# Optimization experiments

Hardware: AMD Instinct MI355X
Metric: run time of the kernel (lower is better)

## Reference

```python
import jax, jax.numpy as jnp
import numpy as np

D_MODEL = 1024
NUM_HEADS = 16
NUM_KV_HEADS = 4
D_K = D_MODEL // NUM_HEADS          # 64
GROUP = NUM_HEADS // NUM_KV_HEADS   # 4
D_KV = D_MODEL // GROUP             # 256


def setup_inputs() -> dict:
    key = jax.random.key(0)
    ks = jax.random.split(key, 12)
    B, S = 2, 2048
    sc = 0.02
    return {
        "query": jax.random.normal(ks[0], (B, S, D_MODEL), jnp.float32),
        "key": jax.random.normal(ks[1], (B, S, D_MODEL), jnp.float32),
        "value": jax.random.normal(ks[2], (B, S, D_MODEL), jnp.float32),
        "w_q": jax.random.normal(ks[3], (D_MODEL, D_MODEL), jnp.float32) * sc,
        "b_q": jnp.zeros((D_MODEL,), jnp.float32),
        "w_k": jax.random.normal(ks[4], (D_KV, D_MODEL), jnp.float32) * sc,
        "b_k": jnp.zeros((D_KV,), jnp.float32),
        "w_v": jax.random.normal(ks[5], (D_KV, D_MODEL), jnp.float32) * sc,
        "b_v": jnp.zeros((D_KV,), jnp.float32),
        "w_o": jax.random.normal(ks[6], (D_MODEL, D_MODEL), jnp.float32) * sc,
        "b_o": jnp.zeros((D_MODEL,), jnp.float32),
    }


def reference(query, key, value, w_q, b_q, w_k, b_k, w_v, b_v, w_o, b_o):
    B, S, _ = query.shape
    # projections (torch Linear: x @ W.T + b)
    Q = query @ w_q.T + b_q            # [B,S,d_model]
    K = key @ w_k.T + b_k              # [B,S,d_kv]
    V = value @ w_v.T + b_v            # [B,S,d_kv]
    # [B, Hkv, G, S, Dk] for Q; [B, Hkv, S, Dk] for K/V.
    # repeat_interleave(group, dim=1) on K/V == sharing each KV head across
    # its group of query heads, so we contract without duplicating K/V.
    Q = Q.reshape(B, S, NUM_KV_HEADS, GROUP, D_K).transpose(0, 2, 3, 1, 4)
    K = K.reshape(B, S, NUM_KV_HEADS, D_K).transpose(0, 2, 1, 3)
    V = V.reshape(B, S, NUM_KV_HEADS, D_K).transpose(0, 2, 1, 3)
    scale = 1.0 / jnp.sqrt(jnp.asarray(D_K, Q.dtype))
    scores = jnp.einsum('bhgsd,bhtd->bhgst', Q, K) * scale  # [B,Hkv,G,S,S]
    attn = jax.nn.softmax(scores, axis=-1)
    out = jnp.einsum('bhgst,bhtd->bhgsd', attn, V)          # [B,Hkv,G,S,Dk]
    # -> [B,S,Hkv*G*Dk] = [B,S,d_model]
    out = out.transpose(0, 3, 1, 2, 4).reshape(B, S, D_MODEL)
    return out @ w_o.T + b_o
```

## Files before the change

kernel.cpp:

```cpp
#include <hip/hip_runtime.h>
#include <hip/hip_bf16.h>
#include <stdint.h>

typedef unsigned short u16;
typedef unsigned int   u32;
typedef short s16x8 __attribute__((ext_vector_type(8)));
typedef u16   u16x4 __attribute__((ext_vector_type(4)));
typedef u16   u16x8 __attribute__((ext_vector_type(8)));
typedef u32   u32x2 __attribute__((ext_vector_type(2)));
typedef u32   u32x4 __attribute__((ext_vector_type(4)));
typedef float f32x4  __attribute__((ext_vector_type(4)));
typedef float f32x16 __attribute__((ext_vector_type(16)));
typedef float f4     __attribute__((ext_vector_type(4)));

#define MFMA(a,b,c)   __builtin_amdgcn_mfma_f32_16x16x32_bf16((a),(b),(c),0,0,0)
#define MFMA32(a,b,c) __builtin_amdgcn_mfma_f32_32x32x16_bf16((a),(b),(c),0,0,0)

__device__ __forceinline__ u16 f2b(float f){
  union { float f; unsigned u; } v; v.f = f;
  unsigned r = v.u + 0x7fffu + ((v.u >> 16) & 1u);
  return (u16)(r >> 16);
}

__device__ __forceinline__ u32 cvtpk(float lo, float hi){
  u32 r;
  asm("v_cvt_pk_bf16_f32 %0, %1, %2" : "=v"(r) : "v"(lo), "v"(hi));
  return r;
}

__device__ __forceinline__ float exp2h(float x){
  float r;
  asm("v_exp_f32 %0, %1" : "=v"(r) : "v"(x));
  return r;
}

__device__ __forceinline__ void gll16(const void* g, void* l){
  __builtin_amdgcn_global_load_lds(
      (const __attribute__((address_space(1))) void*)g,
      (__attribute__((address_space(3))) void*)l, 16, 0, 0);
}

__global__ __launch_bounds__(256) void wcast(const float* __restrict__ wq,
                                             const float* __restrict__ wk,
                                             const float* __restrict__ wv,
                                             const float* __restrict__ wo,
                                             u16* dq, u16* dk, u16* dv, u16* dov){
  int e = (blockIdx.x * 256 + threadIdx.x) * 4;
  const float* s; u16* d; int off;
  if      (e < 1048576){ s = wq; d = dq;  off = 0; }
  else if (e < 1310720){ s = wk; d = dk;  off = 1048576; }
  else if (e < 1572864){ s = wv; d = dv;  off = 1310720; }
  else                 { s = wo; d = dov; off = 1572864; }
  int i = e - off;
  f4 v = *(const f4*)(s + i);
  u32x2 o; o[0] = cvtpk(v[0], v[1]); o[1] = cvtpk(v[2], v[3]);
  *(u32x2*)(d + i) = o;
}

__global__ __launch_bounds__(256) void qkv_gemm(
    const float* __restrict__ qa, const float* __restrict__ ka, const float* __restrict__ va,
    const u16* __restrict__ wq, const u16* __restrict__ wk, const u16* __restrict__ wv,
    const float* __restrict__ bq, const float* __restrict__ bk, const float* __restrict__ bv,
    u16* Qo, u16* Ko, u16* Vto){
  __shared__ u16 As[2][128*32];
  __shared__ u16 Bs[2][128*32];
  const int tid = threadIdx.x, lane = tid & 63, wid = tid >> 6;
  const int bid = blockIdx.x;
  const float* A; const u16* B; const float* bias; int N; float cscale; int bm, bn;
  bool isV = false;
  if (bid < 256)      { A=qa; B=wq; bias=bq; N=1024; cscale=0.18033688011112f; bm=bid>>3;       bn=bid&7; }
  else if (bid < 320) { A=ka; B=wk; bias=bk; N=256;  cscale=1.0f;              bm=(bid-256)>>1; bn=(bid-256)&1; }
  else                { A=va; B=wv; bias=bv; N=256;  cscale=1.0f;              bm=(bid-320)>>1; bn=(bid-320)&1; isV = true; }
  const int wr = wid >> 1, wc = wid & 1;
  const int r15 = lane & 15, kg = lane >> 4;

  const u16*  Bg = B + (size_t)bn * 128 * 1024;
  const float* Ag = A + (size_t)bm * 128 * 1024;
  f32x4 acc[4][4] = {};

  #pragma unroll
  for (int i = 0; i < 2; i++){
    int cc = wid + i*4, row = cc*16 + (lane >> 2);
    gll16((const char*)Bg + ((size_t)row*1024)*2 + (lane & 3)*16, (char*)&Bs[0][0] + cc*1024);
  }
  #pragma unroll
  for (int p = 0; p < 4; p++){
    int c = tid + p*256, row = c >> 3, c4 = (c & 7) << 2;
    f4 v = *(const f4*)(Ag + (size_t)row*1024 + c4);
    u32x2 o; o[0] = cvtpk(v[0], v[1]); o[1] = cvtpk(v[2], v[3]);
    *(u32x2*)&As[0][row*32 + c4] = o;
  }
  __syncthreads();

  for (int k0 = 0; k0 < 1024; k0 += 32){
    const int cur = (k0 >> 5) & 1;
    const bool pf = (k0 + 32) < 1024;
    f4 areg[4];
    if (pf){
      #pragma unroll
      for (int i = 0; i < 2; i++){
        int cc = wid + i*4, row = cc*16 + (lane >> 2);
        gll16((const char*)Bg + ((size_t)row*1024 + k0 + 32)*2 + (lane & 3)*16,
              (char*)&Bs[cur^1][0] + cc*1024);
      }
      #pragma unroll
      for (int p = 0; p < 4; p++){
        int c = tid + p*256, row = c >> 3, c4 = (c & 7) << 2;
        areg[p] = *(const f4*)(Ag + (size_t)row*1024 + k0 + 32 + c4);
      }
    }
    s16x8 af[4], bf[4];
    #pragma unroll
    for (int i = 0; i < 4; i++)
      af[i] = *(const s16x8*)&As[cur][(wr*64 + i*16 + r15)*32 + kg*8];
    #pragma unroll
    for (int j = 0; j < 4; j++)
      bf[j] = *(const s16x8*)&Bs[cur][(wc*64 + j*16 + r15)*32 + kg*8];
    __builtin_amdgcn_s_setprio(1);
    #pragma unroll
    for (int i = 0; i < 4; i++)
      #pragma unroll
      for (int j = 0; j < 4; j++)
        acc[i][j] = MFMA(af[i], bf[j], acc[i][j]);
    __builtin_amdgcn_s_setprio(0);
    if (pf){
      #pragma unroll
      for (int p = 0; p < 4; p++){
        int c = tid + p*256, row = c >> 3, c4 = (c & 7) << 2;
        u32x2 o; o[0] = cvtpk(areg[p][0], areg[p][1]); o[1] = cvtpk(areg[p][2], areg[p][3]);
        *(u32x2*)&As[cur^1][row*32 + c4] = o;
      }
    }
    __syncthreads();
  }

  if (isV){
    #pragma unroll
    for (int i = 0; i < 4; i++){
      int row0 = bm*128 + wr*64 + i*16 + kg*4;
      int bb = row0 >> 11, t = row0 & 2047;
      #pragma unroll
      for (int j = 0; j < 4; j++){
        int col = bn*128 + wc*64 + j*16 + r15;
        float bj = bias[col];
        u16x4 vv;
        #pragma unroll
        for (int r = 0; r < 4; r++) vv[r] = f2b(acc[i][j][r] + bj);
        *(u16x4*)&Vto[((size_t)(bb*256 + col) << 11) + t] = vv;
      }
    }
  } else {
    u16* C = (bid < 256) ? Qo : Ko;
    #pragma unroll
    for (int i = 0; i < 4; i++){
      int row = bm*128 + wr*64 + i*16 + kg*4;
      #pragma unroll
      for (int j = 0; j < 4; j++){
        int col = bn*128 + wc*64 + j*16 + r15;
        float bj = bias[col];
        #pragma unroll
        for (int r = 0; r < 4; r++)
          C[(size_t)(row + r)*N + col] = f2b((acc[i][j][r] + bj) * cscale);
      }
    }
  }
}

__global__ __launch_bounds__(256) void gemm_o(const u16* __restrict__ Aw,
                                              const u16* __restrict__ Bw,
                                              const float* __restrict__ bias,
                                              float* __restrict__ Cv){
  __shared__ u16 As[2][128*32];
  __shared__ u16 Bs[2][128*32];
  const int tid = threadIdx.x, lane = tid & 63, wid = tid >> 6;
  const int bm = blockIdx.x >> 3, bn = blockIdx.x & 7;
  const int wr = wid >> 1, wc = wid & 1;
  const int r15 = lane & 15, kg = lane >> 4;
  const u16* Ag = Aw + (size_t)bm * 128 * 1024;
  const u16* Bg = Bw + (size_t)bn * 128 * 1024;
  f32x4 acc[4][4] = {};

  auto stage = [&](int buf, int k0){
    #pragma unroll
    for (int i = 0; i < 2; i++){
      int cc = wid + i*4, row = cc*16 + (lane >> 2);
      gll16((const char*)Ag + ((size_t)row*1024 + k0)*2 + (lane & 3)*16, (char*)&As[buf][0] + cc*1024);
      gll16((const char*)Bg + ((size_t)row*1024 + k0)*2 + (lane & 3)*16, (char*)&Bs[buf][0] + cc*1024);
    }
  };
  stage(0, 0);
  __syncthreads();
  for (int k0 = 0; k0 < 1024; k0 += 32){
    const int cur = (k0 >> 5) & 1;
    if (k0 + 32 < 1024) stage(cur ^ 1, k0 + 32);
    s16x8 af[4], bf[4];
    #pragma unroll
    for (int i = 0; i < 4; i++)
      af[i] = *(const s16x8*)&As[cur][(wr*64 + i*16 + r15)*32 + kg*8];
    #pragma unroll
    for (int j = 0; j < 4; j++)
      bf[j] = *(const s16x8*)&Bs[cur][(wc*64 + j*16 + r15)*32 + kg*8];
    __builtin_amdgcn_s_setprio(1);
    #pragma unroll
    for (int i = 0; i < 4; i++)
      #pragma unroll
      for (int j = 0; j < 4; j++)
        acc[i][j] = MFMA(af[i], bf[j], acc[i][j]);
    __builtin_amdgcn_s_setprio(0);
    __syncthreads();
  }
  #pragma unroll
  for (int i = 0; i < 4; i++){
    int row = bm*128 + wr*64 + i*16 + kg*4;
    #pragma unroll
    for (int j = 0; j < 4; j++){
      int col = bn*128 + wc*64 + j*16 + r15;
      float bj = bias[col];
      #pragma unroll
      for (int r = 0; r < 4; r++)
        Cv[(size_t)(row + r)*1024 + col] = acc[i][j][r] + bj;
    }
  }
}

__global__ __launch_bounds__(512, 4) void attn_fwd(const u16* __restrict__ Qp,
                                                   const u16* __restrict__ Kp,
                                                   const u16* __restrict__ Vt,
                                                   u16* __restrict__ Op){
  __shared__ u16 Ks[2][2][64*64];
  __shared__ u16 Vs[2][2][64*64];
  const int tid = threadIdx.x, lane = tid & 63, w = tid >> 6;
  const int wg = w & 3, g = w >> 2;
  const int bx = blockIdx.x;
  const int qt = bx & 15, h = (bx >> 4) & 15, b = bx >> 8;
  const int kvh = h >> 2;
  const int l31 = lane & 31, hh = lane >> 5;
  const int srow = lane >> 3;
  const int scol16 = ((lane & 7) ^ srow) << 4;

  const size_t qrow0 = (size_t)(b*2048 + qt*128 + wg*32 + l31) << 10;
  s16x8 qf[4];
  #pragma unroll
  for (int db = 0; db < 4; db++)
    qf[db] = *(const s16x8*)(Qp + qrow0 + h*64 + db*16 + hh*8);

  f32x16 oacc[2] = {};
  const f32x16 ZERO = {};
  float lsum = 0.f;

  auto stage = [&](int buf, int t0){
    #pragma unroll
    for (int i = 0; i < 2; i++){
      int cc = wg + i*4;
      int row = cc*8 + srow;
      const u16* ksrc = Kp + ((size_t)(b*2048 + t0 + row) << 8) + kvh*64;
      gll16((const char*)ksrc + scol16, (char*)&Ks[g][buf][0] + cc*1024);
      const u16* vsrc = Vt + ((size_t)((b*4 + kvh)*64 + row) << 11) + t0;
      gll16((const char*)vsrc + scol16, (char*)&Vs[g][buf][0] + cc*1024);
    }
  };

  stage(0, g*64);
  __syncthreads();

  for (int it = 0; it < 16; it++){
    const int cur = it & 1;
    if (it + 1 < 16) stage(cur ^ 1, (2*(it + 1) + g)*64);

    f32x16 sacc[2];
    __builtin_amdgcn_s_setprio(1);
    #pragma unroll
    for (int kb2 = 0; kb2 < 2; kb2++){
      #pragma unroll
      for (int db = 0; db < 4; db++){
        int row = kb2*32 + l31;
        int slot = (db*2 + hh) ^ (row & 7);
        s16x8 kf = *(const s16x8*)((const char*)&Ks[g][cur][0] + row*128 + slot*16);
        sacc[kb2] = MFMA32(kf, qf[db], (db == 0) ? ZERO : sacc[kb2]);
      }
    }
    __builtin_amdgcn_s_setprio(0);

    u32 W[2][4][2];
    #pragma unroll
    for (int kb2 = 0; kb2 < 2; kb2++){
      float p[16];
      #pragma unroll
      for (int r = 0; r < 16; r++){
        p[r] = exp2h(sacc[kb2][r]);
        lsum += p[r];
      }
      #pragma unroll
      for (int a = 0; a < 4; a++){
        W[kb2][a][0] = cvtpk(p[4*a + 0], p[4*a + 1]);
        W[kb2][a][1] = cvtpk(p[4*a + 2], p[4*a + 3]);
      }
    }

    s16x8 pa[4];
    #pragma unroll
    for (int kq = 0; kq < 4; kq++){
      const int kb2 = kq >> 1, c = kq & 1;
      u32x4 dw;
      #pragma unroll
      for (int pp = 0; pp < 2; pp++){
        u32 x = W[kb2][2*c][pp], y = W[kb2][2*c + 1][pp];
        asm volatile("v_permlane32_swap_b32 %0, %1" : "+v"(x), "+v"(y));
        dw[pp] = x; dw[2 + pp] = y;
      }
      pa[kq] = *(const s16x8*)&dw;
    }

    __builtin_amdgcn_s_setprio(1);
    #pragma unroll
    for (int dblk = 0; dblk < 2; dblk++){
      #pragma unroll
      for (int kq = 0; kq < 4; kq++){
        int row = dblk*32 + l31;
        int slot = (kq*2 + hh) ^ (row & 7);
        s16x8 vf = *(const s16x8*)((const char*)&Vs[g][cur][0] + row*128 + slot*16);
        oacc[dblk] = MFMA32(pa[kq], vf, oacc[dblk]);
      }
    }
    __builtin_amdgcn_s_setprio(0);
    __syncthreads();
  }

  float rsum = lsum + __shfl_xor(lsum, 32, 64);
  float* Om = (float*)&Ks[0][0][0];
  float* Ls = (float*)&Vs[0][0][0];
  if (g == 1){
    #pragma unroll
    for (int reg = 0; reg < 16; reg++){
      int q = (reg & 3) + 4*hh + 8*(reg >> 2);
      #pragma unroll
      for (int dblk = 0; dblk < 2; dblk++)
        Om[(wg*32 + q)*64 + dblk*32 + l31] = oacc[dblk][reg];
    }
    if (hh == 0) Ls[wg*32 + l31] = rsum;
  }
  __syncthreads();
  if (g == 0){
    rsum += Ls[wg*32 + l31];
    float rinv = __builtin_amdgcn_rcpf(rsum);
    const size_t obase = (size_t)(b*2048 + qt*128 + wg*32) << 10;
    #pragma unroll
    for (int reg = 0; reg < 16; reg++){
      const int qrow = (reg & 3) + 4*hh + 8*(reg >> 2);
      float rq = __shfl(rinv, qrow, 64);
      #pragma unroll
      for (int dblk = 0; dblk < 2; dblk++){
        float v = (oacc[dblk][reg] + Om[(wg*32 + qrow)*64 + dblk*32 + l31]) * rq;
        Op[obase + ((size_t)qrow << 10) + h*64 + dblk*32 + l31] = f2b(v);
      }
    }
  }
}

extern "C" void kernel_launch(void* const* d_in, const int* in_sizes, int n_in,
                              void* d_out, int out_size, void* d_ws, size_t ws_size,
                              hipStream_t stream){
  const float* query = (const float*)d_in[0];
  const float* key   = (const float*)d_in[1];
  const float* value = (const float*)d_in[2];
  const float* w_q   = (const float*)d_in[3];
  const float* b_q   = (const float*)d_in[4];
  const float* w_k   = (const float*)d_in[5];
  const float* b_k   = (const float*)d_in[6];
  const float* w_v   = (const float*)d_in[7];
  const float* b_v   = (const float*)d_in[8];
  const float* w_o   = (const float*)d_in[9];
  const float* b_o   = (const float*)d_in[10];

  char* ws = (char*)d_ws;
  size_t off = 0;
  u16* wqb = (u16*)(ws + off); off += (size_t)1024*1024*2;
  u16* wkb = (u16*)(ws + off); off += (size_t)256*1024*2;
  u16* wvb = (u16*)(ws + off); off += (size_t)256*1024*2;
  u16* wob = (u16*)(ws + off); off += (size_t)1024*1024*2;
  u16* Qw  = (u16*)(ws + off); off += (size_t)4096*1024*2;
  u16* Kw  = (u16*)(ws + off); off += (size_t)4096*256*2;
  u16* Vtw = (u16*)(ws + off); off += (size_t)4096*256*2;
  u16* AOw = (u16*)(ws + off); off += (size_t)4096*1024*2;

  wcast<<<2560, 256, 0, stream>>>(w_q, w_k, w_v, w_o, wqb, wkb, wvb, wob);

  qkv_gemm<<<384, 256, 0, stream>>>(query, key, value, wqb, wkb, wvb,
                                    b_q, b_k, b_v, Qw, Kw, Vtw);

  attn_fwd<<<512, 512, 0, stream>>>(Qw, Kw, Vtw, AOw);

  gemm_o<<<256, 256, 0, stream>>>(AOw, wob, b_o, (float*)d_out);
}
```

Measured before the change: 110.3 us.

## Halve QKV GEMM M-tile to 64 rows and remap block order for XCD locality

The QKV projection GEMM now uses 64x128 output tiles instead of 128x128, doubling the grid from 384 to 768 blocks so more CUs (256 on MI355X) have work and the tail is smaller. Each thread loads and converts one 8-float A chunk per k-step. Both qkv_gemm and gemm_o also permute the block index so that consecutive logical tiles land on the same XCD, aiming at better L2 reuse of shared A/B tiles. The smaller M-tile lowers MFMA work per B-tile load, so B weight traffic per output rises.

```diff
diff --git a/kernel.cpp b/kernel.cpp
--- a/kernel.cpp
+++ b/kernel.cpp
@@ -62,40 +62,42 @@
     const u16* __restrict__ wq, const u16* __restrict__ wk, const u16* __restrict__ wv,
     const float* __restrict__ bq, const float* __restrict__ bk, const float* __restrict__ bv,
     u16* Qo, u16* Ko, u16* Vto){
-  __shared__ u16 As[2][128*32];
+  __shared__ u16 As[2][64*32];
   __shared__ u16 Bs[2][128*32];
   const int tid = threadIdx.x, lane = tid & 63, wid = tid >> 6;
-  const int bid = blockIdx.x;
+  const int lb = (blockIdx.x & 7) * 96 + (blockIdx.x >> 3);
   const float* A; const u16* B; const float* bias; int N; float cscale; int bm, bn;
   bool isV = false;
-  if (bid < 256)      { A=qa; B=wq; bias=bq; N=1024; cscale=0.18033688011112f; bm=bid>>3;       bn=bid&7; }
-  else if (bid < 320) { A=ka; B=wk; bias=bk; N=256;  cscale=1.0f;              bm=(bid-256)>>1; bn=(bid-256)&1; }
-  else                { A=va; B=wv; bias=bv; N=256;  cscale=1.0f;              bm=(bid-320)>>1; bn=(bid-320)&1; isV = true; }
+  if (lb < 512)      { A=qa; B=wq; bias=bq; N=1024; cscale=0.18033688011112f; bm=lb>>3;         bn=lb&7; }
+  else if (lb < 640) { A=ka; B=wk; bias=bk; N=256;  cscale=1.0f;              bm=(lb-512)>>1;   bn=(lb-512)&1; }
+  else               { A=va; B=wv; bias=bv; N=256;  cscale=1.0f;              bm=(lb-640)>>1;   bn=(lb-640)&1; isV = true; }
   const int wr = wid >> 1, wc = wid & 1;
   const int r15 = lane & 15, kg = lane >> 4;
 
   const u16*  Bg = B + (size_t)bn * 128 * 1024;
-  const float* Ag = A + (size_t)bm * 128 * 1024;
-  f32x4 acc[4][4] = {};
+  const float* Ag = A + (size_t)bm * 64 * 1024;
+  f32x4 acc[2][4] = {};
+
+  const int arow = tid >> 2, ac8 = (tid & 3) << 3;
 
   #pragma unroll
   for (int i = 0; i < 2; i++){
     int cc = wid + i*4, row = cc*16 + (lane >> 2);
     gll16((const char*)Bg + ((size_t)row*1024)*2 + (lane & 3)*16, (char*)&Bs[0][0] + cc*1024);
   }
-  #pragma unroll
-  for (int p = 0; p < 4; p++){
-    int c = tid + p*256, row = c >> 3, c4 = (c & 7) << 2;
-    f4 v = *(const f4*)(Ag + (size_t)row*1024 + c4);
-    u32x2 o; o[0] = cvtpk(v[0], v[1]); o[1] = cvtpk(v[2], v[3]);
-    *(u32x2*)&As[0][row*32 + c4] = o;
+  {
+    f4 v0 = *(const f4*)(Ag + (size_t)arow*1024 + ac8);
+    f4 v1 = *(const f4*)(Ag + (size_t)arow*1024 + ac8 + 4);
+    u32x4 o; o[0]=cvtpk(v0[0],v0[1]); o[1]=cvtpk(v0[2],v0[3]);
+             o[2]=cvtpk(v1[0],v1[1]); o[3]=cvtpk(v1[2],v1[3]);
+    *(u32x4*)&As[0][arow*32 + ac8] = o;
   }
   __syncthreads();
 
   for (int k0 = 0; k0 < 1024; k0 += 32){
     const int cur = (k0 >> 5) & 1;
     const bool pf = (k0 + 32) < 1024;
-    f4 areg[4];
+    f4 a0, a1;
     if (pf){
       #pragma unroll
       for (int i = 0; i < 2; i++){
@@ -103,41 +105,35 @@
         gll16((const char*)Bg + ((size_t)row*1024 + k0 + 32)*2 + (lane & 3)*16,
               (char*)&Bs[cur^1][0] + cc*1024);
       }
-      #pragma unroll
-      for (int p = 0; p < 4; p++){
-        int c = tid + p*256, row = c >> 3, c4 = (c & 7) << 2;
-        areg[p] = *(const f4*)(Ag + (size_t)row*1024 + k0 + 32 + c4);
-      }
-    }
-    s16x8 af[4], bf[4];
-    #pragma unroll
-    for (int i = 0; i < 4; i++)
-      af[i] = *(const s16x8*)&As[cur][(wr*64 + i*16 + r15)*32 + kg*8];
+      a0 = *(const f4*)(Ag + (size_t)arow*1024 + k0 + 32 + ac8);
+      a1 = *(const f4*)(Ag + (size_t)arow*1024 + k0 + 32 + ac8 + 4);
+    }
+    s16x8 af[2], bf[4];
+    #pragma unroll
+    for (int i = 0; i < 2; i++)
+      af[i] = *(const s16x8*)&As[cur][(wr*32 + i*16 + r15)*32 + kg*8];
     #pragma unroll
     for (int j = 0; j < 4; j++)
       bf[j] = *(const s16x8*)&Bs[cur][(wc*64 + j*16 + r15)*32 + kg*8];
     __builtin_amdgcn_s_setprio(1);
     #pragma unroll
-    for (int i = 0; i < 4; i++)
+    for (int i = 0; i < 2; i++)
       #pragma unroll
       for (int j = 0; j < 4; j++)
         acc[i][j] = MFMA(af[i], bf[j], acc[i][j]);
     __builtin_amdgcn_s_setprio(0);
     if (pf){
-      #pragma unroll
-      for (int p = 0; p < 4; p++){
-        int c = tid + p*256, row = c >> 3, c4 = (c & 7) << 2;
-        u32x2 o; o[0] = cvtpk(areg[p][0], areg[p][1]); o[1] = cvtpk(areg[p][2], areg[p][3]);
-        *(u32x2*)&As[cur^1][row*32 + c4] = o;
-      }
+      u32x4 o; o[0]=cvtpk(a0[0],a0[1]); o[1]=cvtpk(a0[2],a0[3]);
+               o[2]=cvtpk(a1[0],a1[1]); o[3]=cvtpk(a1[2],a1[3]);
+      *(u32x4*)&As[cur^1][arow*32 + ac8] = o;
     }
     __syncthreads();
   }
 
   if (isV){
     #pragma unroll
-    for (int i = 0; i < 4; i++){
-      int row0 = bm*128 + wr*64 + i*16 + kg*4;
+    for (int i = 0; i < 2; i++){
+      int row0 = bm*64 + wr*32 + i*16 + kg*4;
       int bb = row0 >> 11, t = row0 & 2047;
       #pragma unroll
       for (int j = 0; j < 4; j++){
@@ -150,10 +146,10 @@
       }
     }
   } else {
-    u16* C = (bid < 256) ? Qo : Ko;
-    #pragma unroll
-    for (int i = 0; i < 4; i++){
-      int row = bm*128 + wr*64 + i*16 + kg*4;
+    u16* C = (lb < 512) ? Qo : Ko;
+    #pragma unroll
+    for (int i = 0; i < 2; i++){
+      int row = bm*64 + wr*32 + i*16 + kg*4;
       #pragma unroll
       for (int j = 0; j < 4; j++){
         int col = bn*128 + wc*64 + j*16 + r15;
@@ -173,7 +169,8 @@
   __shared__ u16 As[2][128*32];
   __shared__ u16 Bs[2][128*32];
   const int tid = threadIdx.x, lane = tid & 63, wid = tid >> 6;
-  const int bm = blockIdx.x >> 3, bn = blockIdx.x & 7;
+  const int lb = (blockIdx.x & 7) * 32 + (blockIdx.x >> 3);
+  const int bm = lb >> 3, bn = lb & 7;
   const int wr = wid >> 1, wc = wid & 1;
   const int r15 = lane & 15, kg = lane >> 4;
   const u16* Ag = Aw + (size_t)bm * 128 * 1024;
@@ -385,7 +382,7 @@
 
   wcast<<<2560, 256, 0, stream>>>(w_q, w_k, w_v, w_o, wqb, wkb, wvb, wob);
 
-  qkv_gemm<<<384, 256, 0, stream>>>(query, key, value, wqb, wkb, wvb,
+  qkv_gemm<<<768, 256, 0, stream>>>(query, key, value, wqb, wkb, wvb,
                                     b_q, b_k, b_v, Qw, Kw, Vtw);
 
   attn_fwd<<<512, 512, 0, stream>>>(Qw, Kw, Vtw, AOw);
```

After: 102.6 us. 7.0% less time.
